# Kernel tuning notes

Hardware: AMD Instinct MI355X
Metric: run time of the kernel (lower is better)

Reference implementation:

```python
import jax, jax.numpy as jnp
from jax import lax
import numpy as np

B, C, H, W, OUTC, KS = 4, 64, 128, 128, 64, 3
N = KS * KS
PAD = 1
STRIDE = 1


def conv2d(x, w, b, stride, pad):
    out = lax.conv_general_dilated(x, w, (stride, stride), ((pad, pad), (pad, pad)),
                                   dimension_numbers=('NCHW', 'OIHW', 'NCHW'))
    if b is not None:
        out = out + b[None, :, None, None]
    return out


def setup_inputs() -> dict:
    key = jax.random.key(0)
    k = jax.random.split(key, 8)
    f = jnp.float32

    def w_init(kk, shape, fan_in, scale=1.0):
        return jax.random.normal(kk, shape, f) * (scale / np.sqrt(fan_in))

    return {
        'x': jax.random.normal(k[0], (B, C, H, W), f),
        'ref': jax.random.normal(k[1], (B, C, H, W), f),
        'w_cd': w_init(k[2], (C, 2 * C, 1, 1), 2 * C),
        'b_cd': jnp.zeros((C,), f),
        'w_p': w_init(k[3], (2 * N, C, 3, 3), C * 9, 0.1),  # small offsets, keeps sampling stable
        'b_p': jnp.zeros((2 * N,), f),
        'w_m': w_init(k[4], (N, C, 3, 3), C * 9),
        'b_m': jnp.zeros((N,), f),
        'w_c': w_init(k[5], (N * C, C, 3, 3), C * 9),
        'b_c': jnp.zeros((N * C,), f),
        'w_conv': w_init(k[6], (OUTC, C, KS, KS), C * KS * KS),
    }


def deform_forward(x, ref, w_cd, b_cd, w_p, b_p, w_m, b_m, w_c, b_c, w_conv):
    b, c, h, w = x.shape
    fused = conv2d(jnp.concatenate([x, ref], axis=1), w_cd, b_cd, 1, 0)
    offset = conv2d(fused, w_p, b_p, STRIDE, 1)             # [b, 2N, h, w]
    m = jax.nn.sigmoid(conv2d(fused, w_m, b_m, STRIDE, 1))  # [b, N, h, w]
    c_off = jnp.tanh(conv2d(fused, w_c, b_c, STRIDE, 1))    # [b, N*c, h, w]

    xp = jnp.pad(x, ((0, 0), (0, 0), (PAD, PAD), (PAD, PAD)))
    Hp, Wp = h + 2 * PAD, w + 2 * PAD

    # kernel-relative grid p_n (first N entries = rows, last N = cols)
    r = jnp.arange(-(KS - 1) // 2, (KS - 1) // 2 + 1)
    pnx, pny = jnp.meshgrid(r, r, indexing='ij')
    p_n = jnp.concatenate([pnx.ravel(), pny.ravel()]).reshape(1, 2 * N, 1, 1)
    # base grid p_0 starts at 1 because of the zero padding
    gx, gy = jnp.meshgrid(jnp.arange(1, h * STRIDE + 1, STRIDE),
                          jnp.arange(1, w * STRIDE + 1, STRIDE), indexing='ij')
    p_0 = jnp.concatenate([jnp.broadcast_to(gx[None, None], (1, N, h, w)),
                           jnp.broadcast_to(gy[None, None], (1, N, h, w))], axis=1)
    p = (p_0 + p_n).astype(offset.dtype) + offset           # [b, 2N, h, w]
    p = p.transpose(0, 2, 3, 1)                             # [b, h, w, 2N]

    q_lt = jnp.floor(lax.stop_gradient(p))
    q_rb = q_lt + 1

    def clampq(q):
        return jnp.concatenate([jnp.clip(q[..., :N], 0, Hp - 1),
                                jnp.clip(q[..., N:], 0, Wp - 1)], axis=-1).astype(jnp.int32)

    q_lt = clampq(q_lt)
    q_rb = clampq(q_rb)
    q_lb = jnp.concatenate([q_lt[..., :N], q_rb[..., N:]], axis=-1)
    q_rt = jnp.concatenate([q_rb[..., :N], q_lt[..., N:]], axis=-1)
    p = jnp.concatenate([jnp.clip(p[..., :N], 0, Hp - 1),
                         jnp.clip(p[..., N:], 0, Wp - 1)], axis=-1)

    def gweight(q, sx, sy):
        qx = q[..., :N].astype(p.dtype)
        qy = q[..., N:].astype(p.dtype)
        return (1 + sx * (qx - p[..., :N])) * (1 + sy * (qy - p[..., N:]))

    g_lt = gweight(q_lt, 1, 1)
    g_rb = gweight(q_rb, -1, -1)
    g_lb = gweight(q_lb, 1, -1)
    g_rt = gweight(q_rt, -1, 1)

    x_flat = xp.reshape(b, c, Hp * Wp)

    def get_x_q(q):
        idx = q[..., :N] * Wp + q[..., N:]                  # [b, h, w, N]
        xq = jnp.take_along_axis(x_flat, idx.reshape(b, 1, -1), axis=2)
        return xq.reshape(b, c, h, w, N)

    x_off = (g_lt[:, None] * get_x_q(q_lt) + g_rb[:, None] * get_x_q(q_rb)
             + g_lb[:, None] * get_x_q(q_lb) + g_rt[:, None] * get_x_q(q_rt))

    # color deformation: [b, N*c, h, w] -> [b, c, h, w, N]
    x_off = x_off + c_off.reshape(b, c, N, h, w).transpose(0, 1, 3, 4, 2)
    # modulation broadcast over channels
    x_off = x_off * m.transpose(0, 2, 3, 1)[:, None]

    # [b,c,h,w,N] -> [b,c,h*ks,w*ks] with N = (kernel_row, kernel_col)
    x_off = x_off.reshape(b, c, h, w, KS, KS).transpose(0, 1, 2, 4, 3, 5)
    x_off = x_off.reshape(b, c, h * KS, w * KS)
    return conv2d(x_off, w_conv, None, KS, 0)


def reference(x, ref, w_cd, b_cd, w_p, b_p, w_m, b_m, w_c, b_c, w_conv):
    return deform_forward(x, ref, w_cd, b_cd, w_p, b_p, w_m, b_m, w_c, b_c, w_conv)
```

## Files before the change

kernel.cpp:

```cpp
#include <hip/hip_runtime.h>
#include <hip/hip_fp16.h>


typedef __attribute__((ext_vector_type(8))) __bf16 bf16x8;
typedef __attribute__((ext_vector_type(16))) float f32x16;
#define MFMA32(a, b, c) __builtin_amdgcn_mfma_f32_32x32x16_bf16((a), (b), (c), 0, 0, 0)

#define WS_AC    0
#define WS_APM   368640
#define WS_ACONV 387072
#define WS_F2    436224

struct f2pair { float x, y; };

__device__ __forceinline__ unsigned short f2bf(float f) {
    unsigned u = __float_as_uint(f);
    return (unsigned short)((u + 0x7FFFu + ((u >> 16) & 1u)) >> 16);
}
__device__ __forceinline__ float fast_rcp(float x) {
#if __has_builtin(__builtin_amdgcn_rcpf)
    return __builtin_amdgcn_rcpf(x);
#else
    return 1.0f / x;
#endif
}
__device__ __forceinline__ float fast_tanh(float x) {
    float t = __expf(2.0f * x);
    return 1.0f - 2.0f * fast_rcp(t + 1.0f);
}
__device__ __forceinline__ float fast_sigmoid(float x) {
    return fast_rcp(1.0f + __expf(-x));
}
__device__ __forceinline__ float comp4(const float4& v, int e) {
    return (e == 0) ? v.x : (e == 1) ? v.y : (e == 2) ? v.z : v.w;
}

__device__ __forceinline__ uint4 stage_load64(const unsigned short* f2b, int h,
                                              int px0, int chunk, int tid) {
    int tap = chunk >> 1;
    int dh = tap / 3 - 1, dw = tap % 3 - 1;
    int hs = h + dh;
    int kg = tid >> 6, px = tid & 63;
    int cg = (chunk & 1) * 4 + kg;
    int wsrc = px0 + px + dw;
    uint4 pk = {0u, 0u, 0u, 0u};
    if (((unsigned)hs < 128u) && ((unsigned)wsrc < 128u))
        pk = *(const uint4*)(f2b + (((size_t)cg << 14) + (hs << 7) + wsrc) * 8);
    return pk;
}
__device__ __forceinline__ void stage_write64(char* Bst, uint4 pk, int tid) {
    int kg = tid >> 6, px = tid & 63;
    *(uint4*)(Bst + ((kg >> 1) * 2 + (px >> 5)) * 1024
                  + ((px & 31) + 32 * (kg & 1)) * 16) = pk;
}

__global__ __launch_bounds__(256, 4)
void k2_fused(const float* __restrict__ x, const float* __restrict__ ref,
              const float* __restrict__ b_cd, const float* __restrict__ w_c,
              const float* __restrict__ w_p, const float* __restrict__ w_m,
              const float* __restrict__ w_conv, const float* __restrict__ w_cd,
              unsigned short* __restrict__ ws) {
    __shared__ __align__(16) char B0[32768];
    __shared__ __align__(16) unsigned short WcdL[8192];
    const int tid = threadIdx.x, l = tid & 63, w = tid >> 6;
    const int b = blockIdx.y, p0 = blockIdx.x * 128;
    const int rl31 = l & 31, kh8 = (l >> 5) * 8;

    {
        int gtid = (blockIdx.y * 128 + blockIdx.x) * 256 + tid;
        #pragma unroll 1
        for (int i = gtid; i < 428032; i += 131072) {
            float val;
            if (i < WS_APM) {
                int t = i, jj = t & 7, lx = (t >> 3) & 63, r = t >> 9;
                int ks = r % 36, gmt = r / 36;
                int row = gmt * 32 + (lx & 31);
                int kp = ks * 16 + (lx >> 5) * 8 + jj, tap = kp >> 6, ci = kp & 63;
                val = (row < 576) ? w_c[row * 576 + ci * 9 + tap] : 0.0f;
            } else if (i < WS_ACONV) {
                int t = i - WS_APM, jj = t & 7, lx = (t >> 3) & 63, ks = t >> 9;
                int row = lx & 31;
                int kp = ks * 16 + (lx >> 5) * 8 + jj, tap = kp >> 6, ci = kp & 63;
                val = (row < 18) ? w_p[row * 576 + ci * 9 + tap]
                    : (row < 27) ? w_m[(row - 18) * 576 + ci * 9 + tap] : 0.0f;
            } else {
                int t = i - WS_ACONV, jj = t & 7, lx = (t >> 3) & 63, r = t >> 9;
                int gks = r % 40, ocT2 = r / 40;
                int oc = ocT2 * 32 + (lx & 31);
                int krow = gks * 16 + (lx >> 5) * 8 + jj;
                val = (krow < 576) ? w_conv[oc * 576 + krow] : 0.0f;
            }
            ws[i] = f2bf(val);
        }
    }
    #pragma unroll
    for (int i = tid; i < 8192; i += 256) WcdL[i] = f2bf(w_cd[i]);

    #pragma unroll
    for (int it = 0; it < 2; ++it) {
        int task = it * 256 + tid;
        int kg = task >> 5, pxg = task & 31;
        const float* src = (kg < 8) ? x : ref;
        int kbase = (kg & 7) * 8;
        const float* sp = src + (((size_t)b * 64 + kbase) << 14) + p0 + pxg * 4;
        float4 v0 = *(const float4*)(sp);
        float4 v1 = *(const float4*)(sp + (1 << 14));
        float4 v2 = *(const float4*)(sp + (2 << 14));
        float4 v3 = *(const float4*)(sp + (3 << 14));
        float4 v4 = *(const float4*)(sp + (4 << 14));
        float4 v5 = *(const float4*)(sp + (5 << 14));
        float4 v6 = *(const float4*)(sp + (6 << 14));
        float4 v7 = *(const float4*)(sp + (7 << 14));
        char* bb = B0 + ((kg >> 1) * 4 + (pxg >> 3)) * 1024 + 32 * (kg & 1) * 16;
        #pragma unroll
        for (int e = 0; e < 4; ++e) {
            uint4 pk;
            pk.x = (unsigned)f2bf(comp4(v0, e)) | ((unsigned)f2bf(comp4(v1, e)) << 16);
            pk.y = (unsigned)f2bf(comp4(v2, e)) | ((unsigned)f2bf(comp4(v3, e)) << 16);
            pk.z = (unsigned)f2bf(comp4(v4, e)) | ((unsigned)f2bf(comp4(v5, e)) << 16);
            pk.w = (unsigned)f2bf(comp4(v6, e)) | ((unsigned)f2bf(comp4(v7, e)) << 16);
            *(uint4*)(bb + ((pxg & 7) * 4 + e) * 16) = pk;
        }
    }
    __syncthreads();

    f32x16 a0, a1;
    #pragma unroll
    for (int r = 0; r < 16; ++r) { a0[r] = 0.0f; a1[r] = 0.0f; }
    const unsigned short* A0 = WcdL + rl31 * 128 + kh8;
    #pragma unroll
    for (int s = 0; s < 8; ++s) {
        bf16x8 bf = *(bf16x8*)(B0 + ((s * 4 + w) * 64 + l) * 16);
        bf16x8 x0 = *(const bf16x8*)(A0 + s * 16);
        bf16x8 x1 = *(const bf16x8*)(A0 + 32 * 128 + s * 16);
        a0 = MFMA32(x0, bf, a0);
        a1 = MFMA32(x1, bf, a1);
    }
    unsigned short* f2 = ws + WS_F2 + ((size_t)b << 20);
    int px = p0 + w * 32 + rl31;
    int h4 = (l >> 5) * 4;
    #pragma unroll
    for (int t = 0; t < 2; ++t)
        #pragma unroll
        for (int q = 0; q < 4; ++q) {
            ushort4 st;
            float v0 = (t ? a1[q * 4 + 0] : a0[q * 4 + 0]) + b_cd[t * 32 + 8 * q + h4 + 0];
            float v1 = (t ? a1[q * 4 + 1] : a0[q * 4 + 1]) + b_cd[t * 32 + 8 * q + h4 + 1];
            float v2 = (t ? a1[q * 4 + 2] : a0[q * 4 + 2]) + b_cd[t * 32 + 8 * q + h4 + 2];
            float v3 = (t ? a1[q * 4 + 3] : a0[q * 4 + 3]) + b_cd[t * 32 + 8 * q + h4 + 3];
            st.x = f2bf(v0); st.y = f2bf(v1); st.z = f2bf(v2); st.w = f2bf(v3);
            *(ushort4*)(f2 + ((size_t)((t * 4 + q) << 14) + px) * 8 + h4) = st;
        }
}

__global__ __launch_bounds__(256, 4)
void k3_main(const float* __restrict__ x, const float* __restrict__ b_c,
             const float* __restrict__ b_p, const float* __restrict__ b_m,
             const unsigned short* __restrict__ wsbf, float* __restrict__ out) {
    __shared__ __align__(16) char lds[36096];
    char* Bst0 = lds;
    char* Bst1 = lds + 4096;
    char* Amod = lds + 8192;
    float* uL = (float*)(lds + 8192);
    char* tbl = lds + 24576;
    float* bcL = (float*)(lds + 33792);

    const int tid = threadIdx.x, l = tid & 63, w = tid >> 6;
    const int lh = l >> 5, l31 = l & 31;
    const int id = blockIdx.x;
    const int hbLin = (id & 7) * 128 + (id >> 3);
    const int half = hbLin & 1, b = (hbLin >> 1) & 3, h = hbLin >> 3;
    const int px0 = half * 64;
    const unsigned short* f2b = wsbf + WS_F2 + ((size_t)b << 20);
    const float* xb = x + (((size_t)b * 64) << 14);
    const int ocT = w >> 1, nT2 = w & 1;

    for (int i = tid; i < 576; i += 256) bcL[i] = b_c[i];

    {
        f32x16 pm;
        #pragma unroll
        for (int r = 0; r < 16; ++r) pm[r] = 0.0f;
        stage_write64(Bst0, stage_load64(f2b, h, px0, 0, tid), tid);
        __syncthreads();
        #pragma unroll 1
        for (int it = 0; it < 18; ++it) {
            char* cur = (it & 1) ? Bst1 : Bst0;
            char* nxt = (it & 1) ? Bst0 : Bst1;
            uint4 pk;
            if (it < 17) pk = stage_load64(f2b, h, px0, it + 1, tid);
            if (w < 2) {
                #pragma unroll
                for (int s = 0; s < 2; ++s) {
                    int ks = it * 2 + s;
                    bf16x8 bf = *(bf16x8*)(cur + ((s * 2 + w) * 64 + l) * 16);
                    bf16x8 apm = *(const bf16x8*)(wsbf + WS_APM + ((ks * 64 + l) << 3));
                    pm = MFMA32(apm, bf, pm);
                }
            }
            if (it < 17) stage_write64(nxt, pk, tid);
            __syncthreads();
        }
        if (w < 2) {
            int pxp = w * 32 + l31;
            #pragma unroll
            for (int reg = 0; reg < 16; ++reg) {
                int rl = (reg & 3) + 8 * (reg >> 2) + 4 * lh;
                uL[rl * 64 + pxp] = pm[reg];
            }
        }
        __syncthreads();
    }

    #pragma unroll 1
    for (int i = tid; i < 576; i += 256) {
        int n = i >> 6, px = i & 63;
        float offr = uL[n * 64 + px] + b_p[n];
        float offc = uL[(9 + n) * 64 + px] + b_p[9 + n];
        float mraw = uL[(18 + n) * 64 + px] + b_m[n];
        int nr = n / 3, nc = n - nr * 3;
        float pr = (float)(h + nr) + offr;
        float pc = (float)(px0 + px + nc) + offc;
        float flr = floorf(pr), flc = floorf(pc);
        float prc = fminf(fmaxf(pr, 0.0f), 129.0f);
        float pcc = fminf(fmaxf(pc, 0.0f), 129.0f);
        float q0r = fminf(fmaxf(flr, 0.0f), 129.0f);
        float q1r = fminf(fmaxf(flr + 1.0f, 0.0f), 129.0f);
        int ir0 = (int)q0r, ir1 = (int)q1r;
        bool vr0 = (ir0 >= 1) && (ir0 <= 128), vr1 = (ir1 >= 1) && (ir1 <= 128);
        float wr0 = vr0 ? (1.0f + q0r - prc) : 0.0f;
        float wr1 = vr1 ? (1.0f - (q1r - prc)) : 0.0f;
        float q0c = fminf(fmaxf(flc, 0.0f), 129.0f);
        float q1c = fminf(fmaxf(flc + 1.0f, 0.0f), 129.0f);
        int ic0 = (int)q0c, ic1 = (int)q1c;
        bool vc0 = (ic0 >= 1) && (ic0 <= 128), vc1 = (ic1 >= 1) && (ic1 <= 128);
        float wc0 = vc0 ? (1.0f + q0c - pcc) : 0.0f;
        float wc1 = vc1 ? (1.0f - (q1c - pcc)) : 0.0f;
        int cx0 = ic0 - 1, cx1 = ic1 - 1;
        int base = min(max(cx0, 0), 126);
        float ws0 = ((base == cx0) && vc0 ? wc0 : 0.0f)
                  + ((base == cx1) && vc1 ? wc1 : 0.0f);
        float ws1 = ((base + 1 == cx0) && vc0 ? wc0 : 0.0f)
                  + ((base + 1 == cx1) && vc1 ? wc1 : 0.0f);
        int rx0 = min(max(ir0 - 1, 0), 127), rx1 = min(max(ir1 - 1, 0), 127);
        uint4 rec;
        rec.x = (unsigned)__half_as_ushort(__float2half(wr0 * ws0))
              | ((unsigned)__half_as_ushort(__float2half(wr0 * ws1)) << 16);
        rec.y = (unsigned)__half_as_ushort(__float2half(wr1 * ws0))
              | ((unsigned)__half_as_ushort(__float2half(wr1 * ws1)) << 16);
        rec.z = (unsigned)(unsigned short)(rx0 * 128 + base)
              | ((unsigned)(unsigned short)(rx1 * 128 + base) << 16);
        rec.w = __float_as_uint(fast_sigmoid(mraw));
        *(uint4*)(tbl + (px * 9 + n) * 16) = rec;
    }
    __syncthreads();

    f32x16 oa;
    #pragma unroll
    for (int r = 0; r < 16; ++r) oa[r] = 0.0f;

    #pragma unroll 1
    for (int p = 0; p < 5; ++p) {
        const int mt = p * 4 + w;
        f32x16 acc[2];
        #pragma unroll
        for (int j = 0; j < 2; ++j)
            #pragma unroll
            for (int r = 0; r < 16; ++r) acc[j][r] = 0.0f;

        stage_write64(Bst0, stage_load64(f2b, h, px0, 0, tid), tid);
        __syncthreads();
        #pragma unroll 1
        for (int it = 0; it < 18; ++it) {
            char* cur = (it & 1) ? Bst1 : Bst0;
            char* nxt = (it & 1) ? Bst0 : Bst1;
            uint4 pk;
            if (it < 17) pk = stage_load64(f2b, h, px0, it + 1, tid);
            #pragma unroll
            for (int s = 0; s < 2; ++s) {
                const int ks = it * 2 + s;
                bf16x8 bf0 = *(bf16x8*)(cur + ((s * 2 + 0) * 64 + l) * 16);
                bf16x8 bf1 = *(bf16x8*)(cur + ((s * 2 + 1) * 64 + l) * 16);
                bf16x8 af = *(const bf16x8*)(wsbf + WS_AC
                                + (((mt * 36 + ks) * 64 + l) << 3));
                acc[0] = MFMA32(af, bf0, acc[0]);
                acc[1] = MFMA32(af, bf1, acc[1]);
            }
            if (it < 17) stage_write64(nxt, pk, tid);
            __syncthreads();
        }

        const int rowbase = mt * 32;
        #pragma unroll
        for (int j = 0; j < 2; ++j) {
            const int pxe = j * 32 + l31;
            if (rowbase < 576) {
                #pragma unroll
                for (int reg = 0; reg < 16; ++reg) {
                    int rl = (reg & 3) + 8 * (reg >> 2) + 4 * lh;
                    int row = rowbase + rl;
                    int c = row / 9, n = row - c * 9;
                    float uv = acc[j][reg] + bcL[row];
                    float t = fast_tanh(uv);
                    uint4 rec = *(const uint4*)(tbl + (pxe * 9 + n) * 16);
                    float w0 = __half2float(__ushort_as_half((unsigned short)(rec.x & 0xffffu)));
                    float w1 = __half2float(__ushort_as_half((unsigned short)(rec.x >> 16)));
                    float w2 = __half2float(__ushort_as_half((unsigned short)(rec.y & 0xffffu)));
                    float w3 = __half2float(__ushort_as_half((unsigned short)(rec.y >> 16)));
                    int i0 = (int)(rec.z & 0xffffu);
                    int i1 = (int)(rec.z >> 16);
                    float mval = __uint_as_float(rec.w);
                    const float* xp = xb + ((size_t)c << 14);
                    f2pair v0 = *(const f2pair*)(xp + i0);
                    f2pair v1 = *(const f2pair*)(xp + i1);
                    float samp = w0 * v0.x + w1 * v0.y + w2 * v1.x + w3 * v1.y;
                    acc[j][reg] = mval * (samp + t);
                    if ((reg & 3) == 3) __builtin_amdgcn_sched_barrier(0);
                }
            } else {
                #pragma unroll
                for (int reg = 0; reg < 16; ++reg) acc[j][reg] = 0.0f;
            }
        }

        __syncthreads();
        #pragma unroll
        for (int j = 0; j < 2; ++j) {
            #pragma unroll
            for (int reg = 0; reg < 16; ++reg) {
                int rl = (reg & 3) + 8 * (reg >> 2) + 4 * lh;
                int k = w * 32 + rl;
                *(unsigned short*)(Amod + ((k >> 4) * 2 + j) * 1024
                        + (l31 + 32 * ((k >> 3) & 1)) * 16 + (k & 7) * 2)
                    = f2bf(acc[j][reg]);
            }
        }
        __syncthreads();
        #pragma unroll
        for (int ks8 = 0; ks8 < 8; ++ks8) {
            bf16x8 af = *(const bf16x8*)(wsbf + WS_ACONV
                            + (((ocT * 40 + p * 8 + ks8) * 64 + l) << 3));
            bf16x8 bf = *(bf16x8*)(Amod + (ks8 * 2 + nT2) * 1024 + l * 16);
            oa = MFMA32(af, bf, oa);
        }
    }

    float* ob = out + (((size_t)b * 64) << 14) + (h << 7) + px0 + nT2 * 32 + l31;
    #pragma unroll
    for (int reg = 0; reg < 16; ++reg) {
        int rl = (reg & 3) + 8 * (reg >> 2) + 4 * lh;
        int oc = ocT * 32 + rl;
        ob[(size_t)oc << 14] = oa[reg];
    }
}

extern "C" void kernel_launch(void* const* d_in, const int* in_sizes, int n_in,
                              void* d_out, int out_size, void* d_ws, size_t ws_size,
                              hipStream_t stream) {
    const float* x      = (const float*)d_in[0];
    const float* ref    = (const float*)d_in[1];
    const float* w_cd   = (const float*)d_in[2];
    const float* b_cd   = (const float*)d_in[3];
    const float* w_p    = (const float*)d_in[4];
    const float* b_p    = (const float*)d_in[5];
    const float* w_m    = (const float*)d_in[6];
    const float* b_m    = (const float*)d_in[7];
    const float* w_c    = (const float*)d_in[8];
    const float* b_c    = (const float*)d_in[9];
    const float* w_conv = (const float*)d_in[10];
    float* out = (float*)d_out;
    unsigned short* wsbf = (unsigned short*)d_ws;

    hipLaunchKernelGGL(k2_fused, dim3(128, 4), dim3(256), 0, stream,
                       x, ref, b_cd, w_c, w_p, w_m, w_conv, w_cd, wsbf);
    hipLaunchKernelGGL(k3_main, dim3(1024), dim3(256), 0, stream,
                       x, b_c, b_p, b_m, wsbf, out);
}
```

Baseline: 234.3 us.

## Stage full f2 halo tile in LDS once and drop per-pass double-buffered reloads

The kernel now loads the whole 3-row by 66-column halo of the fused feature map for all channel groups into LDS once per block. Previously it re-streamed each tap chunk from global memory through a double buffer, with a barrier per step, six times (the offset/mask pass plus five c_off passes). B fragments are now read straight from the halo tile with tap-shifted addressing, removing the per-step syncs and repeated global traffic. Idle waves 2-3 now compute their part of the first c_off tile alongside the offset/mask GEMM, and the table layout is transposed to n-major. LDS grows to about 52KB and launch bounds drop to 3 blocks per SM, which lowers occupancy.

```diff
diff --git a/kernel.cpp b/kernel.cpp
--- a/kernel.cpp
+++ b/kernel.cpp
@@ -35,23 +35,13 @@
     return (e == 0) ? v.x : (e == 1) ? v.y : (e == 2) ? v.z : v.w;
 }
 
-__device__ __forceinline__ uint4 stage_load64(const unsigned short* f2b, int h,
-                                              int px0, int chunk, int tid) {
-    int tap = chunk >> 1;
-    int dh = tap / 3 - 1, dw = tap % 3 - 1;
-    int hs = h + dh;
-    int kg = tid >> 6, px = tid & 63;
-    int cg = (chunk & 1) * 4 + kg;
-    int wsrc = px0 + px + dw;
-    uint4 pk = {0u, 0u, 0u, 0u};
-    if (((unsigned)hs < 128u) && ((unsigned)wsrc < 128u))
-        pk = *(const uint4*)(f2b + (((size_t)cg << 14) + (hs << 7) + wsrc) * 8);
-    return pk;
-}
-__device__ __forceinline__ void stage_write64(char* Bst, uint4 pk, int tid) {
-    int kg = tid >> 6, px = tid & 63;
-    *(uint4*)(Bst + ((kg >> 1) * 2 + (px >> 5)) * 1024
-                  + ((px & 31) + 32 * (kg & 1)) * 16) = pk;
+__device__ __forceinline__ bf16x8 readB(const char* F2L, int ks, int nt,
+                                        int lh, int l31) {
+    int tap = ks >> 2;
+    int cg = ((ks >> 1) & 1) * 4 + (ks & 1) * 2 + lh;
+    int hr = tap / 3;
+    int wz = nt * 32 + l31 + tap % 3;
+    return *(bf16x8*)(F2L + ((cg * 3 + hr) * 66 + wz) * 16);
 }
 
 __global__ __launch_bounds__(256, 4)
@@ -153,17 +143,16 @@
         }
 }
 
-__global__ __launch_bounds__(256, 4)
+__global__ __launch_bounds__(256, 3)
 void k3_main(const float* __restrict__ x, const float* __restrict__ b_c,
              const float* __restrict__ b_p, const float* __restrict__ b_m,
              const unsigned short* __restrict__ wsbf, float* __restrict__ out) {
-    __shared__ __align__(16) char lds[36096];
-    char* Bst0 = lds;
-    char* Bst1 = lds + 4096;
-    char* Amod = lds + 8192;
-    float* uL = (float*)(lds + 8192);
-    char* tbl = lds + 24576;
-    float* bcL = (float*)(lds + 33792);
+    __shared__ __align__(16) char lds[53248];
+    char* F2L = lds;
+    char* Amod = lds + 25344;
+    float* uL = (float*)(lds + 25344);
+    char* tbl = lds + 41728;
+    float* bcL = (float*)(lds + 50944);
 
     const int tid = threadIdx.x, l = tid & 63, w = tid >> 6;
     const int lh = l >> 5, l31 = l & 31;
@@ -177,40 +166,49 @@
 
     for (int i = tid; i < 576; i += 256) bcL[i] = b_c[i];
 
-    {
+    #pragma unroll 1
+    for (int i = tid; i < 1584; i += 256) {
+        int wz = i % 66, rc = i / 66;
+        int hr = rc % 3, cg = rc / 3;
+        int hs = h + hr - 1, wsrc = px0 - 1 + wz;
+        uint4 pk = {0u, 0u, 0u, 0u};
+        if (((unsigned)hs < 128u) && ((unsigned)wsrc < 128u))
+            pk = *(const uint4*)(f2b + (((size_t)cg << 14) + (hs << 7) + wsrc) * 8);
+        *(uint4*)(F2L + i * 16) = pk;
+    }
+    __syncthreads();
+
+    f32x16 a0p, a1p;
+    #pragma unroll
+    for (int r = 0; r < 16; ++r) { a0p[r] = 0.0f; a1p[r] = 0.0f; }
+    if (w < 2) {
         f32x16 pm;
         #pragma unroll
         for (int r = 0; r < 16; ++r) pm[r] = 0.0f;
-        stage_write64(Bst0, stage_load64(f2b, h, px0, 0, tid), tid);
-        __syncthreads();
-        #pragma unroll 1
-        for (int it = 0; it < 18; ++it) {
-            char* cur = (it & 1) ? Bst1 : Bst0;
-            char* nxt = (it & 1) ? Bst0 : Bst1;
-            uint4 pk;
-            if (it < 17) pk = stage_load64(f2b, h, px0, it + 1, tid);
-            if (w < 2) {
-                #pragma unroll
-                for (int s = 0; s < 2; ++s) {
-                    int ks = it * 2 + s;
-                    bf16x8 bf = *(bf16x8*)(cur + ((s * 2 + w) * 64 + l) * 16);
-                    bf16x8 apm = *(const bf16x8*)(wsbf + WS_APM + ((ks * 64 + l) << 3));
-                    pm = MFMA32(apm, bf, pm);
-                }
-            }
-            if (it < 17) stage_write64(nxt, pk, tid);
-            __syncthreads();
-        }
-        if (w < 2) {
-            int pxp = w * 32 + l31;
-            #pragma unroll
-            for (int reg = 0; reg < 16; ++reg) {
-                int rl = (reg & 3) + 8 * (reg >> 2) + 4 * lh;
-                uL[rl * 64 + pxp] = pm[reg];
-            }
-        }
-        __syncthreads();
-    }
+        #pragma unroll 4
+        for (int ks = 0; ks < 36; ++ks) {
+            bf16x8 bf = readB(F2L, ks, w, lh, l31);
+            bf16x8 apm = *(const bf16x8*)(wsbf + WS_APM + ((ks * 64 + l) << 3));
+            pm = MFMA32(apm, bf, pm);
+        }
+        int pxp = w * 32 + l31;
+        #pragma unroll
+        for (int reg = 0; reg < 16; ++reg) {
+            int rl = (reg & 3) + 8 * (reg >> 2) + 4 * lh;
+            uL[rl * 64 + pxp] = pm[reg];
+        }
+    } else {
+        #pragma unroll 4
+        for (int ks = 0; ks < 36; ++ks) {
+            bf16x8 bf0 = readB(F2L, ks, 0, lh, l31);
+            bf16x8 bf1 = readB(F2L, ks, 1, lh, l31);
+            bf16x8 af = *(const bf16x8*)(wsbf + WS_AC
+                            + (((w * 36 + ks) * 64 + l) << 3));
+            a0p = MFMA32(af, bf0, a0p);
+            a1p = MFMA32(af, bf1, a1p);
+        }
+    }
+    __syncthreads();
 
     #pragma unroll 1
     for (int i = tid; i < 576; i += 256) {
@@ -251,90 +249,100 @@
         rec.z = (unsigned)(unsigned short)(rx0 * 128 + base)
               | ((unsigned)(unsigned short)(rx1 * 128 + base) << 16);
         rec.w = __float_as_uint(fast_sigmoid(mraw));
-        *(uint4*)(tbl + (px * 9 + n) * 16) = rec;
-    }
-    __syncthreads();
-
-    f32x16 oa;
-    #pragma unroll
-    for (int r = 0; r < 16; ++r) oa[r] = 0.0f;
-
-    #pragma unroll 1
-    for (int p = 0; p < 5; ++p) {
-        const int mt = p * 4 + w;
-        f32x16 acc[2];
-        #pragma unroll
-        for (int j = 0; j < 2; ++j)
-            #pragma unroll
-            for (int r = 0; r < 16; ++r) acc[j][r] = 0.0f;
-
-        stage_write64(Bst0, stage_load64(f2b, h, px0, 0, tid), tid);
-        __syncthreads();
-        #pragma unroll 1
-        for (int it = 0; it < 18; ++it) {
-            char* cur = (it & 1) ? Bst1 : Bst0;
-            char* nxt = (it & 1) ? Bst0 : Bst1;
-            uint4 pk;
-            if (it < 17) pk = stage_load64(f2b, h, px0, it + 1, tid);
-            #pragma unroll
-            for (int s = 0; s < 2; ++s) {
-                const int ks = it * 2 + s;
-                bf16x8 bf0 = *(bf16x8*)(cur + ((s * 2 + 0) * 64 + l) * 16);
-                bf16x8 bf1 = *(bf16x8*)(cur + ((s * 2 + 1) * 64 + l) * 16);
-                bf16x8 af = *(const bf16x8*)(wsbf + WS_AC
-                                + (((mt * 36 + ks) * 64 + l) << 3));
-                acc[0] = MFMA32(af, bf0, acc[0]);
-                acc[1] = MFMA32(af, bf1, acc[1]);
-            }
-            if (it < 17) stage_write64(nxt, pk, tid);
-            __syncthreads();
-        }
-
-        const int rowbase = mt * 32;
-        #pragma unroll
-        for (int j = 0; j < 2; ++j) {
-            const int pxe = j * 32 + l31;
-            if (rowbase < 576) {
-                #pragma unroll
-                for (int reg = 0; reg < 16; ++reg) {
-                    int rl = (reg & 3) + 8 * (reg >> 2) + 4 * lh;
-                    int row = rowbase + rl;
-                    int c = row / 9, n = row - c * 9;
-                    float uv = acc[j][reg] + bcL[row];
-                    float t = fast_tanh(uv);
-                    uint4 rec = *(const uint4*)(tbl + (pxe * 9 + n) * 16);
-                    float w0 = __half2float(__ushort_as_half((unsigned short)(rec.x & 0xffffu)));
-                    float w1 = __half2float(__ushort_as_half((unsigned short)(rec.x >> 16)));
-                    float w2 = __half2float(__ushort_as_half((unsigned short)(rec.y & 0xffffu)));
-                    float w3 = __half2float(__ushort_as_half((unsigned short)(rec.y >> 16)));
-                    int i0 = (int)(rec.z & 0xffffu);
-                    int i1 = (int)(rec.z >> 16);
-                    float mval = __uint_as_float(rec.w);
-                    const float* xp = xb + ((size_t)c << 14);
-                    f2pair v0 = *(const f2pair*)(xp + i0);
-                    f2pair v1 = *(const f2pair*)(xp + i1);
-                    float samp = w0 * v0.x + w1 * v0.y + w2 * v1.x + w3 * v1.y;
-                    acc[j][reg] = mval * (samp + t);
-                    if ((reg & 3) == 3) __builtin_amdgcn_sched_barrier(0);
-                }
-            } else {
-                #pragma unroll
-                for (int reg = 0; reg < 16; ++reg) acc[j][reg] = 0.0f;
-            }
-        }
-
-        __syncthreads();
-        #pragma unroll
-        for (int j = 0; j < 2; ++j) {
+        *(uint4*)(tbl + (n * 64 + px) * 16) = rec;
+    }
+    __syncthreads();
+
+    auto epi = [&](f32x16& a, int j, int rowbase) {
+        const int pxe = j * 32 + l31;
+        if (rowbase < 576) {
             #pragma unroll
             for (int reg = 0; reg < 16; ++reg) {
                 int rl = (reg & 3) + 8 * (reg >> 2) + 4 * lh;
-                int k = w * 32 + rl;
-                *(unsigned short*)(Amod + ((k >> 4) * 2 + j) * 1024
-                        + (l31 + 32 * ((k >> 3) & 1)) * 16 + (k & 7) * 2)
-                    = f2bf(acc[j][reg]);
+                int row = rowbase + rl;
+                int c = row / 9, n = row - c * 9;
+                float uv = a[reg] + bcL[row];
+                float t = fast_tanh(uv);
+                uint4 rec = *(const uint4*)(tbl + (n * 64 + pxe) * 16);
+                float w0 = __half2float(__ushort_as_half((unsigned short)(rec.x & 0xffffu)));
+                float w1 = __half2float(__ushort_as_half((unsigned short)(rec.x >> 16)));
+                float w2 = __half2float(__ushort_as_half((unsigned short)(rec.y & 0xffffu)));
+                float w3 = __half2float(__ushort_as_half((unsigned short)(rec.y >> 16)));
+                int i0 = (int)(rec.z & 0xffffu);
+                int i1 = (int)(rec.z >> 16);
+                float mval = __uint_as_float(rec.w);
+                const float* xp = xb + ((size_t)c << 14);
+                f2pair v0 = *(const f2pair*)(xp + i0);
+                f2pair v1 = *(const f2pair*)(xp + i1);
+                float samp = w0 * v0.x + w1 * v0.y + w2 * v1.x + w3 * v1.y;
+                a[reg] = mval * (samp + t);
+                if ((reg & 3) == 3) __builtin_amdgcn_sched_barrier(0);
             }
-        }
+        } else {
+            #pragma unroll
+            for (int reg = 0; reg < 16; ++reg) a[reg] = 0.0f;
+        }
+    };
+    auto scat = [&](const f32x16& a, int j) {
+        #pragma unroll
+        for (int reg = 0; reg < 16; ++reg) {
+            int rl = (reg & 3) + 8 * (reg >> 2) + 4 * lh;
+            int k = w * 32 + rl;
+            *(unsigned short*)(Amod + ((k >> 4) * 2 + j) * 1024
+                    + (l31 + 32 * ((k >> 3) & 1)) * 16 + (k & 7) * 2)
+                = f2bf(a[reg]);
+        }
+    };
+
+    f32x16 oa;
+    #pragma unroll
+    for (int r = 0; r < 16; ++r) oa[r] = 0.0f;
+
+    if (w < 2) {
+        #pragma unroll 4
+        for (int ks = 0; ks < 36; ++ks) {
+            bf16x8 bf0 = readB(F2L, ks, 0, lh, l31);
+            bf16x8 bf1 = readB(F2L, ks, 1, lh, l31);
+            bf16x8 af = *(const bf16x8*)(wsbf + WS_AC
+                            + (((w * 36 + ks) * 64 + l) << 3));
+            a0p = MFMA32(af, bf0, a0p);
+            a1p = MFMA32(af, bf1, a1p);
+        }
+    }
+    epi(a0p, 0, w * 32);
+    epi(a1p, 1, w * 32);
+    __syncthreads();
+    scat(a0p, 0);
+    scat(a1p, 1);
+    __syncthreads();
+    #pragma unroll
+    for (int ks8 = 0; ks8 < 8; ++ks8) {
+        bf16x8 af = *(const bf16x8*)(wsbf + WS_ACONV
+                        + (((ocT * 40 + ks8) * 64 + l) << 3));
+        bf16x8 bf = *(bf16x8*)(Amod + (ks8 * 2 + nT2) * 1024 + l * 16);
+        oa = MFMA32(af, bf, oa);
+    }
+
+    #pragma unroll 1
+    for (int p = 1; p < 5; ++p) {
+        const int mt = p * 4 + w;
+        f32x16 acc0, acc1;
+        #pragma unroll
+        for (int r = 0; r < 16; ++r) { acc0[r] = 0.0f; acc1[r] = 0.0f; }
+        #pragma unroll 4
+        for (int ks = 0; ks < 36; ++ks) {
+            bf16x8 bf0 = readB(F2L, ks, 0, lh, l31);
+            bf16x8 bf1 = readB(F2L, ks, 1, lh, l31);
+            bf16x8 af = *(const bf16x8*)(wsbf + WS_AC
+                            + (((mt * 36 + ks) * 64 + l) << 3));
+            acc0 = MFMA32(af, bf0, acc0);
+            acc1 = MFMA32(af, bf1, acc1);
+        }
+        epi(acc0, 0, mt * 32);
+        epi(acc1, 1, mt * 32);
+        __syncthreads();
+        scat(acc0, 0);
+        scat(acc1, 1);
         __syncthreads();
         #pragma unroll
         for (int ks8 = 0; ks8 < 8; ++ks8) {
```

Result: slower. 275.5 us (+17.6%).
